# Kernel optimization log

Measured on AMD Instinct MI355X. Metric: run time of the kernel, lower is better.

The kernel has to match this reference:

```python
import jax, jax.numpy as jnp
import numpy as np


def setup_inputs() -> dict:
    key = jax.random.key(0)
    k1, k2, k3, k4, k5 = jax.random.split(key, 5)
    B, Cin, D, H, W = 16, 16, 32, 32, 32
    Cout, Kd = 32, 3
    return {
        "x": jax.random.normal(k1, (B, Cin, D, H, W), dtype=jnp.float32),
        "weight": jax.random.normal(k2, (Cout, Cin, Kd, Kd, Kd), dtype=jnp.float32),
        "conv_bias": jax.random.normal(k3, (Cout,), dtype=jnp.float32),
        "scaling_factor": jax.random.normal(k4, (Cout, 1, 1, 1), dtype=jnp.float32),
        "bias_param": jax.random.normal(k5, (Cout, 1, 1, 1), dtype=jnp.float32),
    }


def reference(x, weight, conv_bias, scaling_factor, bias_param):
    # 3D valid conv, stride 1, NCDHW layout / OIDHW kernel
    y = jax.lax.conv_general_dilated(
        x, weight,
        window_strides=(1, 1, 1),
        padding="VALID",
        dimension_numbers=("NCDHW", "OIDHW", "NCDHW"),
    )
    # per-channel bias, scale, tanh, scale, sigmoid (broadcast over D,H,W)
    y = y + conv_bias[None, :, None, None, None]
    y = jnp.tanh(y * scaling_factor[None]) * bias_param[None]
    return jax.nn.sigmoid(y)
```

## Files before the change

### kernel.cpp

```cpp
#include <hip/hip_runtime.h>

#define NB    16
#define CIN   16
#define COUT  32
#define DIN   32
#define DOUT  30

typedef __attribute__((ext_vector_type(8)))  short        short8;
typedef __attribute__((ext_vector_type(4)))  unsigned int uint4v;
typedef __attribute__((ext_vector_type(16))) float        f32x16;

#define XWS_OFS_SHORTS   28672
#define XWS_PART_SHORTS  8388608
#define WS_NEED          (57344 + 2ull * 16 * 1024 * 1024)

static __device__ __forceinline__ unsigned short f2bf_rne(float f) {
    unsigned int u = __builtin_bit_cast(unsigned int, f);
    u += 0x7fffu + ((u >> 16) & 1u);
    return (unsigned short)(u >> 16);
}
static __device__ __forceinline__ float bf2f(unsigned short s) {
    unsigned int u = ((unsigned int)s) << 16;
    return __builtin_bit_cast(float, u);
}
static __device__ __forceinline__ unsigned int cvt_pk_bf16(float a, float b) {
    unsigned int r;
    asm("v_cvt_pk_bf16_f32 %0, %1, %2" : "=v"(r) : "v"(a), "v"(b));
    return r;
}
static __device__ __forceinline__ void gload_lds16(const short* g, short* l) {
    __builtin_amdgcn_global_load_lds(
        (const __attribute__((address_space(1))) void*)g,
        (__attribute__((address_space(3))) void*)l, 16, 0, 0);
}

__global__ __launch_bounds__(64) void repack_w(const float* __restrict__ wgt,
                                               short* __restrict__ ws) {
    const int s  = blockIdx.x;
    const int l  = threadIdx.x;
    const int co  = l & 31;
    const int ci0 = (l >> 5) * 8;
    short8 vh, vl;
#pragma unroll
    for (int j = 0; j < 8; ++j) {
        float f = wgt[co * (CIN * 27) + (ci0 + j) * 27 + s];
        unsigned short h = f2bf_rne(f);
        vh[j] = (short)h;
        vl[j] = (short)f2bf_rne(f - bf2f(h));
    }
    ((short8*)ws)[s * 64 + l]            = vh;
    ((short8*)ws)[27 * 64 + s * 64 + l]  = vl;
}

__global__ __launch_bounds__(256) void repack_x(const float* __restrict__ x,
                                                short* __restrict__ xws) {
    const int rp  = blockIdx.x * 4 + (threadIdx.x >> 6);
    const int l   = threadIdx.x & 63;
    const int hi8 = l >> 5, w = l & 31;
    const int b   = rp >> 10;
    const int dh  = rp & 1023;
    const int gbase = b * (CIN * 32768) + hi8 * 8 * 32768 + dh * 32 + w;
    float f[8];
#pragma unroll
    for (int j = 0; j < 8; ++j) f[j] = x[gbase + j * 32768];
    uint4v vh, vl;
#pragma unroll
    for (int j = 0; j < 8; j += 2) {
        unsigned int hp = cvt_pk_bf16(f[j], f[j + 1]);
        float b0 = __builtin_bit_cast(float, hp << 16);
        float b1 = __builtin_bit_cast(float, hp & 0xffff0000u);
        unsigned int lp = cvt_pk_bf16(f[j] - b0, f[j + 1] - b1);
        vh[j >> 1] = hp;
        vl[j >> 1] = lp;
    }
    ((uint4v*)xws)[rp * 64 + l]               = vh;
    ((uint4v*)xws)[1048576 + rp * 64 + l]     = vl;
}

__global__ __launch_bounds__(512, 4) void conv3d_mfma_v4(
    const short* __restrict__ xws,
    const short* __restrict__ wsA,
    const float* __restrict__ cbias,
    const float* __restrict__ scal,
    const float* __restrict__ bpar,
    float* __restrict__ out)
{
    __shared__ __align__(16) short sx[2 * 18432];
    __shared__ float sp[96];

    const int htile = blockIdx.x;
    const int dquad = blockIdx.y;
    const int b     = blockIdx.z;

    const int tid  = threadIdx.x;
    const int ww   = tid >> 6;
    const int wd   = ww >> 2;
    const int wy   = ww & 3;
    const int lane = tid & 63;

    if (tid < 32) {
        sp[tid]      = cbias[tid];
        sp[32 + tid] = scal[tid];
        sp[64 + tid] = bpar[tid];
    }

    const int h0 = htile * 4;
    const int d0 = dquad * 4;

#pragma unroll
    for (int t = 0; t < 5; ++t) {
        const int rpl = ww + t * 8;
        if (rpl < 36) {
            const int dz  = rpl / 6;
            const int row = rpl - dz * 6;
            int d_in = d0 + dz; if (d_in > 31) d_in = 31;
            int h_in = h0 + row; if (h_in > 31) h_in = 31;
            const int grp = (b * 32 + d_in) * 32 + h_in;
            gload_lds16(xws + (size_t)grp * 512 + lane * 8, sx + rpl * 512);
            gload_lds16(xws + XWS_PART_SHORTS + (size_t)grp * 512 + lane * 8,
                        sx + 18432 + rpl * 512);
        }
    }
    __syncthreads();

    const int h   = h0 + wy;
    const int dw0 = d0 + 2 * wd;
    if (h >= DOUT || dw0 >= DOUT) return;

    const int n  = lane & 31;
    const int hi = lane >> 5;

    const short* pb[3];
#pragma unroll
    for (int kw = 0; kw < 3; ++kw) {
        int wc = n + kw; if (wc > 31) wc = 31;
        pb[kw] = sx + wd * 6144 + wy * 512 + hi * 256 + wc * 8;
    }

    f32x16 acc0, acc1;
#pragma unroll
    for (int i = 0; i < 16; ++i) { acc0[i] = 0.0f; acc1[i] = 0.0f; }

    const short8* wa = (const short8*)wsA;

    short8 Ah0 = wa[0 * 64 + lane],  Ah1 = wa[9 * 64 + lane],  Ah2 = wa[18 * 64 + lane];
    short8 Al0 = wa[1728 + 0 * 64 + lane], Al1 = wa[1728 + 9 * 64 + lane],
           Al2 = wa[1728 + 18 * 64 + lane];

#pragma unroll
    for (int e = 0; e < 9; ++e) {
        const int kh = e / 3, kw = e - kh * 3;
        const int en = (e < 8) ? e + 1 : 8;
        short8 Anh0 = wa[(0 * 9 + en) * 64 + lane];
        short8 Anh1 = wa[(1 * 9 + en) * 64 + lane];
        short8 Anh2 = wa[(2 * 9 + en) * 64 + lane];
        short8 Anl0 = wa[1728 + (0 * 9 + en) * 64 + lane];
        short8 Anl1 = wa[1728 + (1 * 9 + en) * 64 + lane];
        short8 Anl2 = wa[1728 + (2 * 9 + en) * 64 + lane];

        const short* base = pb[kw] + kh * 512;
        short8 bh = *(const short8*)(base);
        short8 bl = *(const short8*)(base + 18432);
#pragma unroll
        for (int dz = 0; dz < 4; ++dz) {
            const short8 cbh = bh, cbl = bl;
            if (dz < 3) {
                bh = *(const short8*)(base + (dz + 1) * 3072);
                bl = *(const short8*)(base + 18432 + (dz + 1) * 3072);
            }
            __builtin_amdgcn_s_setprio(1);
            if (dz < 3) {
                const short8 ah = (dz == 0) ? Ah0 : (dz == 1) ? Ah1 : Ah2;
                const short8 al = (dz == 0) ? Al0 : (dz == 1) ? Al1 : Al2;
                acc0 = __builtin_amdgcn_mfma_f32_32x32x16_bf16(ah, cbh, acc0, 0, 0, 0);
                acc0 = __builtin_amdgcn_mfma_f32_32x32x16_bf16(ah, cbl, acc0, 0, 0, 0);
                acc0 = __builtin_amdgcn_mfma_f32_32x32x16_bf16(al, cbh, acc0, 0, 0, 0);
            }
            if (dz > 0) {
                const short8 ah = (dz == 1) ? Ah0 : (dz == 2) ? Ah1 : Ah2;
                const short8 al = (dz == 1) ? Al0 : (dz == 2) ? Al1 : Al2;
                acc1 = __builtin_amdgcn_mfma_f32_32x32x16_bf16(ah, cbh, acc1, 0, 0, 0);
                acc1 = __builtin_amdgcn_mfma_f32_32x32x16_bf16(ah, cbl, acc1, 0, 0, 0);
                acc1 = __builtin_amdgcn_mfma_f32_32x32x16_bf16(al, cbh, acc1, 0, 0, 0);
            }
            __builtin_amdgcn_s_setprio(0);
        }
        Ah0 = Anh0; Ah1 = Anh1; Ah2 = Anh2;
        Al0 = Anl0; Al1 = Anl1; Al2 = Anl2;
    }

    if (n < DOUT) {
        const int obase = b * (COUT * DOUT * DOUT * DOUT)
                        + dw0 * (DOUT * DOUT) + h * DOUT + n;
#pragma unroll
        for (int r = 0; r < 16; ++r) {
            const int co = (r & 3) + 8 * (r >> 2) + 4 * hi;
            const float cb = sp[co], sc = sp[32 + co], bp = sp[64 + co];
            {
                float y  = acc0[r] + cb;
                float t  = y * sc;
                float th = 1.0f - 2.0f / (__expf(2.0f * t) + 1.0f);
                float z  = th * bp;
                out[obase + co * (DOUT * DOUT * DOUT)] = 1.0f / (1.0f + __expf(-z));
            }
            {
                float y  = acc1[r] + cb;
                float t  = y * sc;
                float th = 1.0f - 2.0f / (__expf(2.0f * t) + 1.0f);
                float z  = th * bp;
                out[obase + (DOUT * DOUT) + co * (DOUT * DOUT * DOUT)] = 1.0f / (1.0f + __expf(-z));
            }
        }
    }
}

__global__ __launch_bounds__(512) void conv3d_mfma_v1(
    const float* __restrict__ x,
    const short* __restrict__ wsA,
    const float* __restrict__ cbias,
    const float* __restrict__ scal,
    const float* __restrict__ bpar,
    float* __restrict__ out)
{
    __shared__ __align__(16) short sx[2 * 12288];
    __shared__ float sp[96];

    const int htile = blockIdx.x;
    const int dpair = blockIdx.y;
    const int b     = blockIdx.z;

    const int tid  = threadIdx.x;
    const int ww   = tid >> 6;
    const int wd   = ww >> 2;
    const int wy   = ww & 3;
    const int lane = tid & 63;

    if (tid < 32) {
        sp[tid]      = cbias[tid];
        sp[32 + tid] = scal[tid];
        sp[64 + tid] = bpar[tid];
    }

    const int h0 = htile * 4;
    const int d0 = dpair * 2;

    const int xb = b * (CIN * DIN * DIN * DIN);
    for (int c = tid; c < 1536; c += 512) {
        const int w   = c & 31;
        const int hi8 = (c >> 5) & 1;
        const int rr  = c >> 6;
        const int dz  = rr / 6;
        const int row = rr - dz * 6;
        int h_in = h0 + row; if (h_in > 31) h_in = 31;
        const int gbase = xb + (hi8 * 8) * (DIN * DIN * DIN)
                        + (d0 + dz) * (DIN * DIN) + h_in * DIN + w;
        float f[8];
#pragma unroll
        for (int j = 0; j < 8; ++j) f[j] = x[gbase + j * (DIN * DIN * DIN)];
        uint4v vh, vl;
#pragma unroll
        for (int j = 0; j < 8; j += 2) {
            unsigned int hp = cvt_pk_bf16(f[j], f[j + 1]);
            float b0 = __builtin_bit_cast(float, hp << 16);
            float b1 = __builtin_bit_cast(float, hp & 0xffff0000u);
            unsigned int lp = cvt_pk_bf16(f[j] - b0, f[j + 1] - b1);
            vh[j >> 1] = hp;
            vl[j >> 1] = lp;
        }
        const int idx = rr * 64 + hi8 * 32 + w;
        *(uint4v*)(sx + idx * 8)         = vh;
        *(uint4v*)(sx + 12288 + idx * 8) = vl;
    }
    __syncthreads();

    const int h = h0 + wy;
    if (h >= DOUT) return;
    const int d = d0 + wd;

    const int n  = lane & 31;
    const int hi = lane >> 5;

    int wofs[3];
#pragma unroll
    for (int kw = 0; kw < 3; ++kw) {
        int wc = n + kw; if (wc > 31) wc = 31;
        wofs[kw] = hi * 256 + wc * 8;
    }

    f32x16 acc;
#pragma unroll
    for (int i = 0; i < 16; ++i) acc[i] = 0.0f;

    const short8* wa = (const short8*)wsA;
#pragma unroll
    for (int kd = 0; kd < 3; ++kd) {
#pragma unroll
        for (int kh = 0; kh < 3; ++kh) {
            const int rbase = ((wd + kd) * 6 + wy + kh) * 512;
#pragma unroll
            for (int kw = 0; kw < 3; ++kw) {
                const int s = kd * 9 + kh * 3 + kw;
                short8 ah = wa[s * 64 + lane];
                short8 al = wa[1728 + s * 64 + lane];
                short8 bh = *(const short8*)(sx + rbase + wofs[kw]);
                short8 bl = *(const short8*)(sx + 12288 + rbase + wofs[kw]);
                acc = __builtin_amdgcn_mfma_f32_32x32x16_bf16(ah, bh, acc, 0, 0, 0);
                acc = __builtin_amdgcn_mfma_f32_32x32x16_bf16(ah, bl, acc, 0, 0, 0);
                acc = __builtin_amdgcn_mfma_f32_32x32x16_bf16(al, bh, acc, 0, 0, 0);
            }
        }
    }

    if (n < DOUT) {
        const int obase = b * (COUT * DOUT * DOUT * DOUT)
                        + d * (DOUT * DOUT) + h * DOUT + n;
#pragma unroll
        for (int r = 0; r < 16; ++r) {
            const int co = (r & 3) + 8 * (r >> 2) + 4 * hi;
            float y  = acc[r] + sp[co];
            float t  = y * sp[32 + co];
            float th = 1.0f - 2.0f / (__expf(2.0f * t) + 1.0f);
            float z  = th * sp[64 + co];
            float rr = 1.0f / (1.0f + __expf(-z));
            out[obase + co * (DOUT * DOUT * DOUT)] = rr;
        }
    }
}

extern "C" void kernel_launch(void* const* d_in, const int* in_sizes, int n_in,
                              void* d_out, int out_size, void* d_ws, size_t ws_size,
                              hipStream_t stream) {
    const float* x     = (const float*)d_in[0];
    const float* wgt   = (const float*)d_in[1];
    const float* cbias = (const float*)d_in[2];
    const float* scal  = (const float*)d_in[3];
    const float* bpar  = (const float*)d_in[4];
    float* out = (float*)d_out;
    short* ws  = (short*)d_ws;

    hipLaunchKernelGGL(repack_w, dim3(27), dim3(64), 0, stream, wgt, ws);

    if (ws_size >= WS_NEED) {
        short* xws = ws + XWS_OFS_SHORTS;
        hipLaunchKernelGGL(repack_x, dim3(4096), dim3(256), 0, stream, x, xws);
        hipLaunchKernelGGL(conv3d_mfma_v4, dim3(8, 8, NB), dim3(512), 0, stream,
                           xws, ws, cbias, scal, bpar, out);
    } else {
        hipLaunchKernelGGL(conv3d_mfma_v1, dim3(8, 15, NB), dim3(512), 0, stream,
                           x, ws, cbias, scal, bpar, out);
    }
}
```

Before: 144.9 us.

## Give each wave four output depth slices to reuse B fragments across kd

Each block now runs 4 waves instead of 8, and each wave computes 4 output depth slices with 4 accumulators instead of 2. Each loaded LDS B fragment (6 input depths) is reused across up to three kd taps, which cuts LDS reads and weight-register loads per MFMA. The cost is higher register pressure from four 16-wide accumulators and fewer waves per block, which may reduce latency hiding and occupancy.

```diff
diff --git a/kernel.cpp b/kernel.cpp
--- a/kernel.cpp
+++ b/kernel.cpp
@@ -77,7 +77,7 @@
     ((uint4v*)xws)[1048576 + rp * 64 + l]     = vl;
 }
 
-__global__ __launch_bounds__(512, 4) void conv3d_mfma_v4(
+__global__ __launch_bounds__(256, 2) void conv3d_mfma_v5(
     const short* __restrict__ xws,
     const short* __restrict__ wsA,
     const float* __restrict__ cbias,
@@ -89,13 +89,11 @@
     __shared__ float sp[96];
 
     const int htile = blockIdx.x;
-    const int dquad = blockIdx.y;
+    const int dblk  = blockIdx.y;
     const int b     = blockIdx.z;
 
     const int tid  = threadIdx.x;
     const int ww   = tid >> 6;
-    const int wd   = ww >> 2;
-    const int wy   = ww & 3;
     const int lane = tid & 63;
 
     if (tid < 32) {
@@ -105,27 +103,25 @@
     }
 
     const int h0 = htile * 4;
-    const int d0 = dquad * 4;
-
-#pragma unroll
-    for (int t = 0; t < 5; ++t) {
-        const int rpl = ww + t * 8;
-        if (rpl < 36) {
-            const int dz  = rpl / 6;
-            const int row = rpl - dz * 6;
-            int d_in = d0 + dz; if (d_in > 31) d_in = 31;
-            int h_in = h0 + row; if (h_in > 31) h_in = 31;
-            const int grp = (b * 32 + d_in) * 32 + h_in;
-            gload_lds16(xws + (size_t)grp * 512 + lane * 8, sx + rpl * 512);
-            gload_lds16(xws + XWS_PART_SHORTS + (size_t)grp * 512 + lane * 8,
-                        sx + 18432 + rpl * 512);
-        }
+    const int d0 = dblk * 4;
+
+#pragma unroll
+    for (int t = 0; t < 9; ++t) {
+        const int rpl = ww + t * 4;
+        const int dz  = rpl / 6;
+        const int row = rpl - dz * 6;
+        int d_in = d0 + dz; if (d_in > 31) d_in = 31;
+        int h_in = h0 + row; if (h_in > 31) h_in = 31;
+        const int grp = (b * 32 + d_in) * 32 + h_in;
+        gload_lds16(xws + (size_t)grp * 512 + lane * 8, sx + rpl * 512);
+        gload_lds16(xws + XWS_PART_SHORTS + (size_t)grp * 512 + lane * 8,
+                    sx + 18432 + rpl * 512);
     }
     __syncthreads();
 
-    const int h   = h0 + wy;
-    const int dw0 = d0 + 2 * wd;
-    if (h >= DOUT || dw0 >= DOUT) return;
+    const int wy = ww;
+    const int h  = h0 + wy;
+    if (h >= DOUT) return;
 
     const int n  = lane & 31;
     const int hi = lane >> 5;
@@ -134,12 +130,12 @@
 #pragma unroll
     for (int kw = 0; kw < 3; ++kw) {
         int wc = n + kw; if (wc > 31) wc = 31;
-        pb[kw] = sx + wd * 6144 + wy * 512 + hi * 256 + wc * 8;
-    }
-
-    f32x16 acc0, acc1;
-#pragma unroll
-    for (int i = 0; i < 16; ++i) { acc0[i] = 0.0f; acc1[i] = 0.0f; }
+        pb[kw] = sx + wy * 512 + hi * 256 + wc * 8;
+    }
+
+    f32x16 acc0, acc1, acc2, acc3;
+#pragma unroll
+    for (int i = 0; i < 16; ++i) { acc0[i] = 0.0f; acc1[i] = 0.0f; acc2[i] = 0.0f; acc3[i] = 0.0f; }
 
     const short8* wa = (const short8*)wsA;
 
@@ -159,29 +155,35 @@
         short8 Anl2 = wa[1728 + (2 * 9 + en) * 64 + lane];
 
         const short* base = pb[kw] + kh * 512;
-        short8 bh = *(const short8*)(base);
-        short8 bl = *(const short8*)(base + 18432);
-#pragma unroll
-        for (int dz = 0; dz < 4; ++dz) {
-            const short8 cbh = bh, cbl = bl;
-            if (dz < 3) {
-                bh = *(const short8*)(base + (dz + 1) * 3072);
-                bl = *(const short8*)(base + 18432 + (dz + 1) * 3072);
-            }
+#pragma unroll
+        for (int dz = 0; dz < 6; ++dz) {
+            const short8 bh = *(const short8*)(base + dz * 3072);
+            const short8 bl = *(const short8*)(base + 18432 + dz * 3072);
             __builtin_amdgcn_s_setprio(1);
-            if (dz < 3) {
-                const short8 ah = (dz == 0) ? Ah0 : (dz == 1) ? Ah1 : Ah2;
-                const short8 al = (dz == 0) ? Al0 : (dz == 1) ? Al1 : Al2;
-                acc0 = __builtin_amdgcn_mfma_f32_32x32x16_bf16(ah, cbh, acc0, 0, 0, 0);
-                acc0 = __builtin_amdgcn_mfma_f32_32x32x16_bf16(ah, cbl, acc0, 0, 0, 0);
-                acc0 = __builtin_amdgcn_mfma_f32_32x32x16_bf16(al, cbh, acc0, 0, 0, 0);
-            }
-            if (dz > 0) {
-                const short8 ah = (dz == 1) ? Ah0 : (dz == 2) ? Ah1 : Ah2;
-                const short8 al = (dz == 1) ? Al0 : (dz == 2) ? Al1 : Al2;
-                acc1 = __builtin_amdgcn_mfma_f32_32x32x16_bf16(ah, cbh, acc1, 0, 0, 0);
-                acc1 = __builtin_amdgcn_mfma_f32_32x32x16_bf16(ah, cbl, acc1, 0, 0, 0);
-                acc1 = __builtin_amdgcn_mfma_f32_32x32x16_bf16(al, cbh, acc1, 0, 0, 0);
+#pragma unroll
+            for (int t = 0; t < 4; ++t) {
+                const int kd = dz - t;
+                if (kd >= 0 && kd <= 2) {
+                    const short8 ah = (kd == 0) ? Ah0 : (kd == 1) ? Ah1 : Ah2;
+                    const short8 al = (kd == 0) ? Al0 : (kd == 1) ? Al1 : Al2;
+                    if (t == 0) {
+                        acc0 = __builtin_amdgcn_mfma_f32_32x32x16_bf16(ah, bh, acc0, 0, 0, 0);
+                        acc0 = __builtin_amdgcn_mfma_f32_32x32x16_bf16(ah, bl, acc0, 0, 0, 0);
+                        acc0 = __builtin_amdgcn_mfma_f32_32x32x16_bf16(al, bh, acc0, 0, 0, 0);
+                    } else if (t == 1) {
+                        acc1 = __builtin_amdgcn_mfma_f32_32x32x16_bf16(ah, bh, acc1, 0, 0, 0);
+                        acc1 = __builtin_amdgcn_mfma_f32_32x32x16_bf16(ah, bl, acc1, 0, 0, 0);
+                        acc1 = __builtin_amdgcn_mfma_f32_32x32x16_bf16(al, bh, acc1, 0, 0, 0);
+                    } else if (t == 2) {
+                        acc2 = __builtin_amdgcn_mfma_f32_32x32x16_bf16(ah, bh, acc2, 0, 0, 0);
+                        acc2 = __builtin_amdgcn_mfma_f32_32x32x16_bf16(ah, bl, acc2, 0, 0, 0);
+                        acc2 = __builtin_amdgcn_mfma_f32_32x32x16_bf16(al, bh, acc2, 0, 0, 0);
+                    } else {
+                        acc3 = __builtin_amdgcn_mfma_f32_32x32x16_bf16(ah, bh, acc3, 0, 0, 0);
+                        acc3 = __builtin_amdgcn_mfma_f32_32x32x16_bf16(ah, bl, acc3, 0, 0, 0);
+                        acc3 = __builtin_amdgcn_mfma_f32_32x32x16_bf16(al, bh, acc3, 0, 0, 0);
+                    }
+                }
             }
             __builtin_amdgcn_s_setprio(0);
         }
@@ -190,25 +192,23 @@
     }
 
     if (n < DOUT) {
-        const int obase = b * (COUT * DOUT * DOUT * DOUT)
-                        + dw0 * (DOUT * DOUT) + h * DOUT + n;
+        const int obase = b * (COUT * DOUT * DOUT * DOUT) + d0 * (DOUT * DOUT) + h * DOUT + n;
 #pragma unroll
         for (int r = 0; r < 16; ++r) {
             const int co = (r & 3) + 8 * (r >> 2) + 4 * hi;
             const float cb = sp[co], sc = sp[32 + co], bp = sp[64 + co];
-            {
-                float y  = acc0[r] + cb;
-                float t  = y * sc;
-                float th = 1.0f - 2.0f / (__expf(2.0f * t) + 1.0f);
-                float z  = th * bp;
-                out[obase + co * (DOUT * DOUT * DOUT)] = 1.0f / (1.0f + __expf(-z));
-            }
-            {
-                float y  = acc1[r] + cb;
-                float t  = y * sc;
-                float th = 1.0f - 2.0f / (__expf(2.0f * t) + 1.0f);
-                float z  = th * bp;
-                out[obase + (DOUT * DOUT) + co * (DOUT * DOUT * DOUT)] = 1.0f / (1.0f + __expf(-z));
+            const int ob = obase + co * (DOUT * DOUT * DOUT);
+#pragma unroll
+            for (int t = 0; t < 4; ++t) {
+                if (d0 + t < DOUT) {
+                    const float a = (t == 0) ? acc0[r] : (t == 1) ? acc1[r]
+                                  : (t == 2) ? acc2[r] : acc3[r];
+                    float y  = a + cb;
+                    float tt = y * sc;
+                    float th = 1.0f - 2.0f / (__expf(2.0f * tt) + 1.0f);
+                    float z  = th * bp;
+                    out[ob + t * (DOUT * DOUT)] = 1.0f / (1.0f + __expf(-z));
+                }
             }
         }
     }
@@ -343,7 +343,7 @@
     if (ws_size >= WS_NEED) {
         short* xws = ws + XWS_OFS_SHORTS;
         hipLaunchKernelGGL(repack_x, dim3(4096), dim3(256), 0, stream, x, xws);
-        hipLaunchKernelGGL(conv3d_mfma_v4, dim3(8, 8, NB), dim3(512), 0, stream,
+        hipLaunchKernelGGL(conv3d_mfma_v5, dim3(8, 8, NB), dim3(256), 0, stream,
                            xws, ws, cbias, scal, bpar, out);
     } else {
         hipLaunchKernelGGL(conv3d_mfma_v1, dim3(8, 15, NB), dim3(512), 0, stream,
```

Result: no change. 146.2 us (+0.9%).
